# Performance work log

Measured on AMD Instinct MI355X. Metric: run time of the kernel, lower is better.

The kernel has to match this reference:

```python
import jax, jax.numpy as jnp
import numpy as np

D = 1024  # input_dim


def setup_inputs() -> dict:
    key = jax.random.key(0)
    ks = jax.random.split(key, 7)
    s = 1.0 / np.sqrt(D)
    x = jax.random.normal(ks[0], (4, 2048, D), dtype=jnp.float32)
    Wq = jax.random.uniform(ks[1], (D, D), jnp.float32, -s, s)
    bq = jax.random.uniform(ks[2], (D,), jnp.float32, -s, s)
    Wk = jax.random.uniform(ks[3], (D, D), jnp.float32, -s, s)
    bk = jax.random.uniform(ks[4], (D,), jnp.float32, -s, s)
    Wv = jax.random.uniform(ks[5], (D, D), jnp.float32, -s, s)
    bv = jax.random.uniform(ks[6], (D,), jnp.float32, -s, s)
    return {"x": x, "Wq": Wq, "bq": bq, "Wk": Wk, "bk": bk, "Wv": Wv, "bv": bv}


def reference(x, Wq, bq, Wk, bk, Wv, bv):
    # nn.Linear: x @ W.T + b
    q = jnp.einsum('bsd,ed->bse', x, Wq) + bq
    k = jnp.einsum('bsd,ed->bse', x, Wk) + bk
    v = jnp.einsum('bsd,ed->bse', x, Wv) + bv
    scale = 1.0 / jnp.sqrt(jnp.asarray(x.shape[-1], x.dtype))
    scores = jnp.einsum('bqe,bke->bqk', q, k) * scale  # [B,S,S]
    weights = jax.nn.softmax(scores, axis=-1)
    return jnp.einsum('bqk,bke->bqe', weights, v)
```

## Files before the change

kernel.cpp:

```cpp
#include <hip/hip_runtime.h>
#include <hip/hip_bf16.h>
#include <stdint.h>


typedef float f32x4 __attribute__((ext_vector_type(4)));
typedef short s16x8 __attribute__((ext_vector_type(8)));

__device__ __forceinline__ uint16_t f2bf(float f) {
    uint32_t u = __float_as_uint(f);
    u += 0x7fffu + ((u >> 16) & 1u);
    return (uint16_t)(u >> 16);
}

#define GLOAD16(gp, lp)                                                  \
    __builtin_amdgcn_global_load_lds(                                    \
        (const __attribute__((address_space(1))) uint32_t*)(gp),         \
        (__attribute__((address_space(3))) uint32_t*)(lp), 16, 0, 0)


__global__ __launch_bounds__(256, 2) void proj_qkv(
    const uint16_t* __restrict__ xb, const uint16_t* __restrict__ wqb,
    const uint16_t* __restrict__ wkb, const uint16_t* __restrict__ wvb,
    const float* __restrict__ bq, const float* __restrict__ bk,
    const float* __restrict__ bv,
    uint16_t* __restrict__ qb, uint16_t* __restrict__ kb,
    uint16_t* __restrict__ vtb)
{
    __shared__ __attribute__((aligned(16))) uint16_t As[128 * 64];
    __shared__ __attribute__((aligned(16))) uint16_t Bs1[128 * 64];
    __shared__ __attribute__((aligned(16))) uint16_t Bs2[128 * 64];

    const int id = blockIdx.x;
    const bool qk = id < 512;

    const int t = threadIdx.x;
    const int wave = t >> 6, lane = t & 63;
    const int wm = (wave >> 1) * 64, wn = (wave & 1) * 64;
    const int lr = lane & 15;
    const int lr7 = lr & 7;

    long long row0, col0;
    const uint16_t *A, *B1, *B2;
    if (qk) {
        row0 = (long long)(id >> 3) * 128;
        col0 = (long long)(id & 7) * 128;
        A = xb; B1 = wqb; B2 = wkb;
    } else {
        const int vid = id - 512;
        row0 = (long long)(vid & 7) * 128;
        col0 = (long long)(vid >> 3) * 128;
        A = wvb; B1 = xb; B2 = nullptr;
    }

    const uint16_t* gA[4]; const uint16_t* gB1[4]; const uint16_t* gB2[4];
    uint16_t* lA[4]; uint16_t* lB1[4]; uint16_t* lB2[4];
#pragma unroll
    for (int p = 0; p < 4; ++p) {
        const int cs = p * 256 + wave * 64 + lane;
        const int rr = cs >> 3;
        const int kc = ((cs & 7) ^ (rr & 7)) * 8;
        gA[p]  = A  + (row0 + rr) * 1024 + kc;
        gB1[p] = B1 + (col0 + rr) * 1024 + kc;
        if (qk) gB2[p] = B2 + (col0 + rr) * 1024 + kc;
        lA[p]  = As  + (p * 256 + wave * 64) * 8;
        lB1[p] = Bs1 + (p * 256 + wave * 64) * 8;
        lB2[p] = Bs2 + (p * 256 + wave * 64) * 8;
    }

    f32x4 acc1[4][4] = {};
    f32x4 acc2[4][4] = {};

    for (int k0 = 0; k0 < 1024; k0 += 64) {
#pragma unroll
        for (int p = 0; p < 4; ++p) GLOAD16(gA[p] + k0, lA[p]);
#pragma unroll
        for (int p = 0; p < 4; ++p) GLOAD16(gB1[p] + k0, lB1[p]);
        if (qk) {
#pragma unroll
            for (int p = 0; p < 4; ++p) GLOAD16(gB2[p] + k0, lB2[p]);
        }
        __syncthreads();

#pragma unroll
        for (int kk = 0; kk < 2; ++kk) {
            const int lka = ((kk * 4 + (lane >> 4)) ^ lr7) * 8;
            s16x8 a[4], b[4];
#pragma unroll
            for (int i = 0; i < 4; ++i)
                a[i] = *(const s16x8*)(As + (wm + i * 16 + lr) * 64 + lka);
#pragma unroll
            for (int j = 0; j < 4; ++j)
                b[j] = *(const s16x8*)(Bs1 + (wn + j * 16 + lr) * 64 + lka);
#pragma unroll
            for (int i = 0; i < 4; ++i)
#pragma unroll
                for (int j = 0; j < 4; ++j)
                    acc1[i][j] = __builtin_amdgcn_mfma_f32_16x16x32_bf16(
                        a[i], b[j], acc1[i][j], 0, 0, 0);
            if (qk) {
#pragma unroll
                for (int j = 0; j < 4; ++j)
                    b[j] = *(const s16x8*)(Bs2 + (wn + j * 16 + lr) * 64 + lka);
#pragma unroll
                for (int i = 0; i < 4; ++i)
#pragma unroll
                    for (int j = 0; j < 4; ++j)
                        acc2[i][j] = __builtin_amdgcn_mfma_f32_16x16x32_bf16(
                            a[i], b[j], acc2[i][j], 0, 0, 0);
            }
        }
        __syncthreads();
    }

    const int rbase = wm + (lane >> 4) * 4;
    const int cbase = wn + lr;
    if (qk) {
#pragma unroll
        for (int i = 0; i < 4; ++i)
#pragma unroll
            for (int rr = 0; rr < 4; ++rr) {
                const long long row = row0 + rbase + i * 16 + rr;
#pragma unroll
                for (int j = 0; j < 4; ++j) {
                    const long long col = col0 + cbase + j * 16;
                    qb[row * 1024 + col] = f2bf((acc1[i][j][rr] + bq[col]) * 0.03125f);
                    kb[row * 1024 + col] = f2bf(acc2[i][j][rr] + bk[col]);
                }
            }
    } else {
#pragma unroll
        for (int i = 0; i < 4; ++i)
#pragma unroll
            for (int rr = 0; rr < 4; ++rr) {
                const long long row = row0 + rbase + i * 16 + rr;
                const float bb = bv[row];
#pragma unroll
                for (int j = 0; j < 4; ++j) {
                    const long long col = col0 + cbase + j * 16;
                    vtb[row * 8192 + col] = f2bf(acc1[i][j][rr] + bb);
                }
            }
    }
}

__global__ __launch_bounds__(256, 2) void gemm_exp(
    const uint16_t* __restrict__ Q, const uint16_t* __restrict__ Km,
    uint16_t* __restrict__ P, float* __restrict__ sums)
{
    __shared__ __attribute__((aligned(16))) uint16_t As[128 * 64];
    __shared__ __attribute__((aligned(16))) uint16_t Bs1[128 * 64];
    __shared__ __attribute__((aligned(16))) uint16_t Bs2[128 * 64];

    const int z = blockIdx.z;
    const uint16_t* Ab = Q  + (long long)z * 2048 * 1024;
    const uint16_t* Bb = Km + (long long)z * 2048 * 1024;
    uint16_t* Cb = P + (long long)z * 2048 * 2048;
    float* ax = sums + (long long)z * 2048;

    const int t = threadIdx.x;
    const int wave = t >> 6, lane = t & 63;
    const int wm = (wave >> 1) * 64, wn = (wave & 1) * 64;
    const int lr = lane & 15;
    const int lr7 = lr & 7;
    const long long row0  = (long long)blockIdx.x * 128;
    const long long col0a = (long long)blockIdx.y * 256;
    const long long col0b = col0a + 128;

    const uint16_t* gA[4]; const uint16_t* gB1[4]; const uint16_t* gB2[4];
    uint16_t* lA[4]; uint16_t* lB1[4]; uint16_t* lB2[4];
#pragma unroll
    for (int p = 0; p < 4; ++p) {
        const int cs = p * 256 + wave * 64 + lane;
        const int rr = cs >> 3;
        const int kc = ((cs & 7) ^ (rr & 7)) * 8;
        gA[p]  = Ab + (row0  + rr) * 1024 + kc;
        gB1[p] = Bb + (col0a + rr) * 1024 + kc;
        gB2[p] = Bb + (col0b + rr) * 1024 + kc;
        lA[p]  = As  + (p * 256 + wave * 64) * 8;
        lB1[p] = Bs1 + (p * 256 + wave * 64) * 8;
        lB2[p] = Bs2 + (p * 256 + wave * 64) * 8;
    }

    f32x4 acc1[4][4] = {};
    f32x4 acc2[4][4] = {};

    for (int k0 = 0; k0 < 1024; k0 += 64) {
#pragma unroll
        for (int p = 0; p < 4; ++p) GLOAD16(gA[p] + k0, lA[p]);
#pragma unroll
        for (int p = 0; p < 4; ++p) GLOAD16(gB1[p] + k0, lB1[p]);
#pragma unroll
        for (int p = 0; p < 4; ++p) GLOAD16(gB2[p] + k0, lB2[p]);
        __syncthreads();

#pragma unroll
        for (int kk = 0; kk < 2; ++kk) {
            const int lka = ((kk * 4 + (lane >> 4)) ^ lr7) * 8;
            s16x8 a[4], b[4];
#pragma unroll
            for (int i = 0; i < 4; ++i)
                a[i] = *(const s16x8*)(As + (wm + i * 16 + lr) * 64 + lka);
#pragma unroll
            for (int j = 0; j < 4; ++j)
                b[j] = *(const s16x8*)(Bs1 + (wn + j * 16 + lr) * 64 + lka);
#pragma unroll
            for (int i = 0; i < 4; ++i)
#pragma unroll
                for (int j = 0; j < 4; ++j)
                    acc1[i][j] = __builtin_amdgcn_mfma_f32_16x16x32_bf16(
                        a[i], b[j], acc1[i][j], 0, 0, 0);
#pragma unroll
            for (int j = 0; j < 4; ++j)
                b[j] = *(const s16x8*)(Bs2 + (wn + j * 16 + lr) * 64 + lka);
#pragma unroll
            for (int i = 0; i < 4; ++i)
#pragma unroll
                for (int j = 0; j < 4; ++j)
                    acc2[i][j] = __builtin_amdgcn_mfma_f32_16x16x32_bf16(
                        a[i], b[j], acc2[i][j], 0, 0, 0);
        }
        __syncthreads();
    }

    const int rbase = wm + (lane >> 4) * 4;
    const int cbase = wn + lr;
#pragma unroll
    for (int i = 0; i < 4; ++i)
#pragma unroll
        for (int rr = 0; rr < 4; ++rr) {
            const long long row = row0 + rbase + i * 16 + rr;
            float s = 0.f;
#pragma unroll
            for (int j = 0; j < 4; ++j) {
                const long long ca = col0a + cbase + j * 16;
                const long long cb2 = col0b + cbase + j * 16;
                const float va = __expf(acc1[i][j][rr]);
                const float vb = __expf(acc2[i][j][rr]);
                Cb[row * 2048 + ca]  = f2bf(va);
                Cb[row * 2048 + cb2] = f2bf(vb);
                s += va + vb;
            }
            s += __shfl_xor(s, 1);
            s += __shfl_xor(s, 2);
            s += __shfl_xor(s, 4);
            s += __shfl_xor(s, 8);
            if (lr == 0) atomicAdd(&ax[row], s);
        }
}

__global__ __launch_bounds__(256, 2) void gemm_pv(
    const uint16_t* __restrict__ P, const uint16_t* __restrict__ Vt,
    float* __restrict__ Out, const float* __restrict__ sums)
{
    __shared__ __attribute__((aligned(16))) uint16_t As[128 * 64];
    __shared__ __attribute__((aligned(16))) uint16_t Bs[128 * 64];

    const int z = blockIdx.z;
    const uint16_t* Ab = P + (long long)z * 2048 * 2048;
    const uint16_t* Bb = Vt + (long long)z * 2048;
    float* Cb = Out + (long long)z * 2048 * 1024;
    const float* ax = sums + (long long)z * 2048;

    const int t = threadIdx.x;
    const int wave = t >> 6, lane = t & 63;
    const int wm = (wave >> 1) * 64, wn = (wave & 1) * 64;
    const int lr = lane & 15;
    const int lr7 = lr & 7;
    const long long row0 = (long long)blockIdx.x * 128;
    const long long col0 = (long long)blockIdx.y * 128;

    const uint16_t* gA[4]; const uint16_t* gB[4];
    uint16_t* lA[4]; uint16_t* lB[4];
#pragma unroll
    for (int p = 0; p < 4; ++p) {
        const int cs = p * 256 + wave * 64 + lane;
        const int rr = cs >> 3;
        const int kc = ((cs & 7) ^ (rr & 7)) * 8;
        gA[p] = Ab + (row0 + rr) * 2048 + kc;
        gB[p] = Bb + (col0 + rr) * 8192 + kc;
        lA[p] = As + (p * 256 + wave * 64) * 8;
        lB[p] = Bs + (p * 256 + wave * 64) * 8;
    }

    f32x4 acc[4][4] = {};

    for (int k0 = 0; k0 < 2048; k0 += 64) {
#pragma unroll
        for (int p = 0; p < 4; ++p) GLOAD16(gA[p] + k0, lA[p]);
#pragma unroll
        for (int p = 0; p < 4; ++p) GLOAD16(gB[p] + k0, lB[p]);
        __syncthreads();

#pragma unroll
        for (int kk = 0; kk < 2; ++kk) {
            const int lka = ((kk * 4 + (lane >> 4)) ^ lr7) * 8;
            s16x8 a[4], b[4];
#pragma unroll
            for (int i = 0; i < 4; ++i)
                a[i] = *(const s16x8*)(As + (wm + i * 16 + lr) * 64 + lka);
#pragma unroll
            for (int j = 0; j < 4; ++j)
                b[j] = *(const s16x8*)(Bs + (wn + j * 16 + lr) * 64 + lka);
#pragma unroll
            for (int i = 0; i < 4; ++i)
#pragma unroll
                for (int j = 0; j < 4; ++j)
                    acc[i][j] = __builtin_amdgcn_mfma_f32_16x16x32_bf16(
                        a[i], b[j], acc[i][j], 0, 0, 0);
        }
        __syncthreads();
    }

    const int rbase = wm + (lane >> 4) * 4;
    const int cbase = wn + lr;
#pragma unroll
    for (int i = 0; i < 4; ++i)
#pragma unroll
        for (int rr = 0; rr < 4; ++rr) {
            const long long row = row0 + rbase + i * 16 + rr;
            const float linv = __builtin_amdgcn_rcpf(ax[row]);
#pragma unroll
            for (int j = 0; j < 4; ++j) {
                const long long col = col0 + cbase + j * 16;
                Cb[row * 1024 + col] = acc[i][j][rr] * linv;
            }
        }
}

__global__ void cast_all(const float* __restrict__ x, const float* __restrict__ Wq,
                         const float* __restrict__ Wk, const float* __restrict__ Wv,
                         uint16_t* __restrict__ xb, uint16_t* __restrict__ wqb,
                         uint16_t* __restrict__ wkb, uint16_t* __restrict__ wvb,
                         float* __restrict__ sums) {
    const int b = blockIdx.x;
    const float* in;
    uint16_t* out;
    int i;
    if (b < 8192)       { in = x;  out = xb;  i = b * 256 + threadIdx.x; }
    else if (b < 9216)  { in = Wq; out = wqb; i = (b - 8192) * 256 + threadIdx.x; }
    else if (b < 10240) { in = Wk; out = wkb; i = (b - 9216) * 256 + threadIdx.x; }
    else if (b < 11264) { in = Wv; out = wvb; i = (b - 10240) * 256 + threadIdx.x; }
    else {
        int j = (b - 11264) * 256 + threadIdx.x;
        ((float4*)sums)[j] = make_float4(0.f, 0.f, 0.f, 0.f);
        return;
    }
    float4 v = ((const float4*)in)[i];
    ushort4 o = make_ushort4(f2bf(v.x), f2bf(v.y), f2bf(v.z), f2bf(v.w));
    ((ushort4*)out)[i] = o;
}

extern "C" void kernel_launch(void* const* d_in, const int* in_sizes, int n_in,
                              void* d_out, int out_size, void* d_ws, size_t ws_size,
                              hipStream_t stream) {
    const float* x  = (const float*)d_in[0];
    const float* Wq = (const float*)d_in[1];
    const float* bq = (const float*)d_in[2];
    const float* Wk = (const float*)d_in[3];
    const float* bk = (const float*)d_in[4];
    const float* Wv = (const float*)d_in[5];
    const float* bv = (const float*)d_in[6];

    uint8_t* w = (uint8_t*)d_ws;
    uint16_t* xb  = (uint16_t*)w; w += (size_t)8192 * 1024 * 2;
    uint16_t* wqb = (uint16_t*)w; w += (size_t)1024 * 1024 * 2;
    uint16_t* wkb = (uint16_t*)w; w += (size_t)1024 * 1024 * 2;
    uint16_t* wvb = (uint16_t*)w; w += (size_t)1024 * 1024 * 2;
    uint16_t* qb  = (uint16_t*)w; w += (size_t)8192 * 1024 * 2;
    uint16_t* kb  = (uint16_t*)w; w += (size_t)8192 * 1024 * 2;
    uint16_t* vtb = (uint16_t*)w; w += (size_t)8192 * 1024 * 2;
    uint16_t* pb  = (uint16_t*)w; w += (size_t)4 * 2048 * 2048 * 2;
    float*    sums = (float*)w;  w += (size_t)8192 * 4;

    cast_all<<<dim3(11272), dim3(256), 0, stream>>>(x, Wq, Wk, Wv,
                                                    xb, wqb, wkb, wvb, sums);
    proj_qkv<<<dim3(1024), 256, 0, stream>>>(xb, wqb, wkb, wvb, bq, bk, bv,
                                             qb, kb, vtb);
    gemm_exp<<<dim3(16, 8, 4), 256, 0, stream>>>(qb, kb, pb, sums);
    gemm_pv<<<dim3(16, 8, 4), 256, 0, stream>>>(pb, vtb, (float*)d_out, sums);
}
```

Before: 229.7 us.

## Replace GEMM kernels with shared 8-wave double-buffered pipelined GEMM core

Introduces a templated gemm8 core using 512-thread blocks (8 waves), double-buffered LDS with global_load_lds prefetch two tiles ahead, explicit vmcnt waits, split barriers and s_setprio around MFMA clusters. All four GEMM stages (Q/K projection, V^T projection, QK^T+exp, PV) are rebuilt on it with larger 256x256 or 128x256 tiles, and the fused QKV projection is split into separate QK and V kernels. The aim is to overlap memory loads with MFMA work and raise data reuse per block. In exchange it uses more LDS and registers, adds many barriers per k-step, and adds one kernel launch.

```diff
diff --git a/kernel.cpp b/kernel.cpp
--- a/kernel.cpp
+++ b/kernel.cpp
@@ -1,5 +1,4 @@
 #include <hip/hip_runtime.h>
-#include <hip/hip_bf16.h>
 #include <stdint.h>
 
 
@@ -17,228 +16,256 @@
         (const __attribute__((address_space(1))) uint32_t*)(gp),         \
         (__attribute__((address_space(3))) uint32_t*)(lp), 16, 0, 0)
 
-
-__global__ __launch_bounds__(256, 2) void proj_qkv(
-    const uint16_t* __restrict__ xb, const uint16_t* __restrict__ wqb,
-    const uint16_t* __restrict__ wkb, const uint16_t* __restrict__ wvb,
-    const float* __restrict__ bq, const float* __restrict__ bk,
-    const float* __restrict__ bv,
-    uint16_t* __restrict__ qb, uint16_t* __restrict__ kb,
-    uint16_t* __restrict__ vtb)
-{
-    __shared__ __attribute__((aligned(16))) uint16_t As[128 * 64];
-    __shared__ __attribute__((aligned(16))) uint16_t Bs1[128 * 64];
-    __shared__ __attribute__((aligned(16))) uint16_t Bs2[128 * 64];
-
-    const int id = blockIdx.x;
-    const bool qk = id < 512;
-
-    const int t = threadIdx.x;
-    const int wave = t >> 6, lane = t & 63;
-    const int wm = (wave >> 1) * 64, wn = (wave & 1) * 64;
-    const int lr = lane & 15;
-    const int lr7 = lr & 7;
-
-    long long row0, col0;
-    const uint16_t *A, *B1, *B2;
-    if (qk) {
-        row0 = (long long)(id >> 3) * 128;
-        col0 = (long long)(id & 7) * 128;
-        A = xb; B1 = wqb; B2 = wkb;
-    } else {
-        const int vid = id - 512;
-        row0 = (long long)(vid & 7) * 128;
-        col0 = (long long)(vid >> 3) * 128;
-        A = wvb; B1 = xb; B2 = nullptr;
-    }
-
-    const uint16_t* gA[4]; const uint16_t* gB1[4]; const uint16_t* gB2[4];
-    uint16_t* lA[4]; uint16_t* lB1[4]; uint16_t* lB2[4];
-#pragma unroll
-    for (int p = 0; p < 4; ++p) {
-        const int cs = p * 256 + wave * 64 + lane;
+#define FENCE() asm volatile("" ::: "memory")
+#define BAR() do { FENCE(); __builtin_amdgcn_s_barrier(); FENCE(); } while (0)
+
+template <int N> __device__ __forceinline__ void waitv() {
+    if constexpr (N == 8)      asm volatile("s_waitcnt vmcnt(8)" ::: "memory");
+    else if constexpr (N == 6) asm volatile("s_waitcnt vmcnt(6)" ::: "memory");
+    else                       asm volatile("s_waitcnt vmcnt(0)" ::: "memory");
+}
+
+template <int MFRAG>
+__device__ __forceinline__ void gemm8(
+    uint16_t* lds,
+    const uint16_t* __restrict__ Ag, const long long lda,
+    const uint16_t* __restrict__ Bg, const long long ldb,
+    const int NT, f32x4 (&acc)[MFRAG][4])
+{
+    constexpr int BM   = MFRAG * 32;
+    constexpr int AGL  = BM / 64;
+    constexpr int MH   = MFRAG / 2;
+    constexpr int SLOT = (BM + 256) * 64;
+    constexpr int VMN  = AGL + 4;
+
+    const int tid  = threadIdx.x;
+    const int wave = tid >> 6, lane = tid & 63;
+    const int lr   = lane & 15, hi = lane >> 4, lr7 = lane & 7;
+
+    const uint16_t* gA[AGL]; int lA[AGL];
+    const uint16_t* gB[4];   int lB[4];
+#pragma unroll
+    for (int p = 0; p < AGL; ++p) {
+        const int cs = p * 512 + tid;
         const int rr = cs >> 3;
         const int kc = ((cs & 7) ^ (rr & 7)) * 8;
-        gA[p]  = A  + (row0 + rr) * 1024 + kc;
-        gB1[p] = B1 + (col0 + rr) * 1024 + kc;
-        if (qk) gB2[p] = B2 + (col0 + rr) * 1024 + kc;
-        lA[p]  = As  + (p * 256 + wave * 64) * 8;
-        lB1[p] = Bs1 + (p * 256 + wave * 64) * 8;
-        lB2[p] = Bs2 + (p * 256 + wave * 64) * 8;
+        gA[p] = Ag + (long long)rr * lda + kc;
+        lA[p] = (p * 512 + wave * 64) * 8;
     }
-
-    f32x4 acc1[4][4] = {};
-    f32x4 acc2[4][4] = {};
-
-    for (int k0 = 0; k0 < 1024; k0 += 64) {
-#pragma unroll
-        for (int p = 0; p < 4; ++p) GLOAD16(gA[p] + k0, lA[p]);
-#pragma unroll
-        for (int p = 0; p < 4; ++p) GLOAD16(gB1[p] + k0, lB1[p]);
-        if (qk) {
-#pragma unroll
-            for (int p = 0; p < 4; ++p) GLOAD16(gB2[p] + k0, lB2[p]);
-        }
-        __syncthreads();
-
-#pragma unroll
-        for (int kk = 0; kk < 2; ++kk) {
-            const int lka = ((kk * 4 + (lane >> 4)) ^ lr7) * 8;
-            s16x8 a[4], b[4];
-#pragma unroll
-            for (int i = 0; i < 4; ++i)
-                a[i] = *(const s16x8*)(As + (wm + i * 16 + lr) * 64 + lka);
-#pragma unroll
-            for (int j = 0; j < 4; ++j)
-                b[j] = *(const s16x8*)(Bs1 + (wn + j * 16 + lr) * 64 + lka);
-#pragma unroll
-            for (int i = 0; i < 4; ++i)
-#pragma unroll
-                for (int j = 0; j < 4; ++j)
-                    acc1[i][j] = __builtin_amdgcn_mfma_f32_16x16x32_bf16(
-                        a[i], b[j], acc1[i][j], 0, 0, 0);
-            if (qk) {
-#pragma unroll
-                for (int j = 0; j < 4; ++j)
-                    b[j] = *(const s16x8*)(Bs2 + (wn + j * 16 + lr) * 64 + lka);
-#pragma unroll
-                for (int i = 0; i < 4; ++i)
-#pragma unroll
-                    for (int j = 0; j < 4; ++j)
-                        acc2[i][j] = __builtin_amdgcn_mfma_f32_16x16x32_bf16(
-                            a[i], b[j], acc2[i][j], 0, 0, 0);
+#pragma unroll
+    for (int p = 0; p < 4; ++p) {
+        const int cs = p * 512 + tid;
+        const int rr = cs >> 3;
+        const int kc = ((cs & 7) ^ (rr & 7)) * 8;
+        gB[p] = Bg + (long long)rr * ldb + kc;
+        lB[p] = BM * 64 + (p * 512 + wave * 64) * 8;
+    }
+
+    const int wrow = (wave >> 2) * (MFRAG * 16);
+    const int wcol = (wave & 3) * 64;
+    const int arow = (wrow + lr) * 64;
+    const int brow = BM * 64 + (wcol + lr) * 64;
+    const int koff0 = (hi ^ lr7) * 8;
+    const int koff1 = ((4 + hi) ^ lr7) * 8;
+
+#pragma unroll
+    for (int p = 0; p < AGL; ++p) GLOAD16(gA[p], lds + lA[p]);
+#pragma unroll
+    for (int p = 0; p < 4;  ++p) GLOAD16(gB[p], lds + lB[p]);
+#pragma unroll
+    for (int p = 0; p < AGL; ++p) GLOAD16(gA[p] + 64, lds + SLOT + lA[p]);
+#pragma unroll
+    for (int p = 0; p < 4;  ++p) GLOAD16(gB[p] + 64, lds + SLOT + lB[p]);
+    waitv<VMN>();
+    BAR();
+
+    s16x8 a[MH][2], b0[2][2], b1[2][2];
+
+    for (int t = 0; t < NT; ++t) {
+        uint16_t* L = lds + (t & 1) * SLOT;
+        const int k0 = (t + 2) * 64;
+        const bool pf = (t + 2) < NT;
+
+#pragma unroll
+        for (int i = 0; i < MH; ++i) {
+            a[i][0] = *(const s16x8*)(L + arow + i * 1024 + koff0);
+            a[i][1] = *(const s16x8*)(L + arow + i * 1024 + koff1);
+        }
+#pragma unroll
+        for (int j = 0; j < 2; ++j) {
+            b0[j][0] = *(const s16x8*)(L + brow + j * 1024 + koff0);
+            b0[j][1] = *(const s16x8*)(L + brow + j * 1024 + koff1);
+        }
+        BAR();
+        __builtin_amdgcn_s_setprio(1);
+#pragma unroll
+        for (int kk = 0; kk < 2; ++kk)
+#pragma unroll
+            for (int i = 0; i < MH; ++i)
+#pragma unroll
+                for (int j = 0; j < 2; ++j)
+                    acc[i][j] = __builtin_amdgcn_mfma_f32_16x16x32_bf16(
+                        a[i][kk], b0[j][kk], acc[i][j], 0, 0, 0);
+        __builtin_amdgcn_s_setprio(0);
+        BAR();
+
+#pragma unroll
+        for (int j = 0; j < 2; ++j) {
+            b1[j][0] = *(const s16x8*)(L + brow + (2 + j) * 1024 + koff0);
+            b1[j][1] = *(const s16x8*)(L + brow + (2 + j) * 1024 + koff1);
+        }
+        BAR();
+        __builtin_amdgcn_s_setprio(1);
+#pragma unroll
+        for (int kk = 0; kk < 2; ++kk)
+#pragma unroll
+            for (int i = 0; i < MH; ++i)
+#pragma unroll
+                for (int j = 0; j < 2; ++j)
+                    acc[i][2 + j] = __builtin_amdgcn_mfma_f32_16x16x32_bf16(
+                        a[i][kk], b1[j][kk], acc[i][2 + j], 0, 0, 0);
+        __builtin_amdgcn_s_setprio(0);
+        BAR();
+
+#pragma unroll
+        for (int i = 0; i < MH; ++i) {
+            a[i][0] = *(const s16x8*)(L + arow + (MH + i) * 1024 + koff0);
+            a[i][1] = *(const s16x8*)(L + arow + (MH + i) * 1024 + koff1);
+        }
+        if (pf) {
+#pragma unroll
+            for (int p = 0; p < 4; ++p) GLOAD16(gB[p] + k0, L + lB[p]);
+        }
+        BAR();
+        __builtin_amdgcn_s_setprio(1);
+#pragma unroll
+        for (int kk = 0; kk < 2; ++kk)
+#pragma unroll
+            for (int i = 0; i < MH; ++i)
+#pragma unroll
+                for (int j = 0; j < 2; ++j)
+                    acc[MH + i][2 + j] = __builtin_amdgcn_mfma_f32_16x16x32_bf16(
+                        a[i][kk], b1[j][kk], acc[MH + i][2 + j], 0, 0, 0);
+        __builtin_amdgcn_s_setprio(0);
+        BAR();
+
+        if (pf) {
+#pragma unroll
+            for (int p = 0; p < AGL; ++p) GLOAD16(gA[p] + k0, L + lA[p]);
+        }
+        BAR();
+        __builtin_amdgcn_s_setprio(1);
+#pragma unroll
+        for (int kk = 0; kk < 2; ++kk)
+#pragma unroll
+            for (int i = 0; i < MH; ++i)
+#pragma unroll
+                for (int j = 0; j < 2; ++j)
+                    acc[MH + i][j] = __builtin_amdgcn_mfma_f32_16x16x32_bf16(
+                        a[i][kk], b0[j][kk], acc[MH + i][j], 0, 0, 0);
+        __builtin_amdgcn_s_setprio(0);
+        if (pf) waitv<VMN>(); else waitv<0>();
+        BAR();
+    }
+}
+
+__global__ __launch_bounds__(512, 2) void qk_proj8(
+    const uint16_t* __restrict__ xb, const uint16_t* __restrict__ wqb,
+    const uint16_t* __restrict__ wkb, const float* __restrict__ bq,
+    const float* __restrict__ bk, uint16_t* __restrict__ qb,
+    uint16_t* __restrict__ kb)
+{
+    __shared__ __attribute__((aligned(16))) uint16_t lds[2 * 512 * 64];
+    const long long row0 = (long long)blockIdx.x * 256;
+    const bool isQ = blockIdx.y < 4;
+    const long long col0 = (long long)(blockIdx.y & 3) * 256;
+    const uint16_t* W = isQ ? wqb : wkb;
+
+    f32x4 acc[8][4] = {};
+    gemm8<8>(lds, xb + row0 * 1024, 1024, W + col0 * 1024, 1024, 16, acc);
+
+    const float* bias = isQ ? bq : bk;
+    uint16_t* out = isQ ? qb : kb;
+    const float scale = isQ ? 0.03125f : 1.0f;
+
+    const int tid = threadIdx.x;
+    const int wave = tid >> 6, lane = tid & 63;
+    const int lr = lane & 15, hi = lane >> 4;
+    const int wrow = (wave >> 2) * 128, wcol = (wave & 3) * 64;
+#pragma unroll
+    for (int i = 0; i < 8; ++i)
+#pragma unroll
+        for (int rr = 0; rr < 4; ++rr) {
+            const long long row = row0 + wrow + i * 16 + hi * 4 + rr;
+#pragma unroll
+            for (int j = 0; j < 4; ++j) {
+                const long long col = col0 + wcol + j * 16 + lr;
+                out[row * 1024 + col] = f2bf((acc[i][j][rr] + bias[col]) * scale);
             }
         }
-        __syncthreads();
-    }
-
-    const int rbase = wm + (lane >> 4) * 4;
-    const int cbase = wn + lr;
-    if (qk) {
-#pragma unroll
-        for (int i = 0; i < 4; ++i)
-#pragma unroll
-            for (int rr = 0; rr < 4; ++rr) {
-                const long long row = row0 + rbase + i * 16 + rr;
-#pragma unroll
-                for (int j = 0; j < 4; ++j) {
-                    const long long col = col0 + cbase + j * 16;
-                    qb[row * 1024 + col] = f2bf((acc1[i][j][rr] + bq[col]) * 0.03125f);
-                    kb[row * 1024 + col] = f2bf(acc2[i][j][rr] + bk[col]);
-                }
+}
+
+__global__ __launch_bounds__(512, 2) void vt_proj8(
+    const uint16_t* __restrict__ xb, const uint16_t* __restrict__ wvb,
+    const float* __restrict__ bv, uint16_t* __restrict__ vtb)
+{
+    __shared__ __attribute__((aligned(16))) uint16_t lds[2 * 384 * 64];
+    const long long row0 = (long long)blockIdx.x * 128;
+    const long long col0 = (long long)blockIdx.y * 256;
+
+    f32x4 acc[4][4] = {};
+    gemm8<4>(lds, wvb + row0 * 1024, 1024, xb + col0 * 1024, 1024, 16, acc);
+
+    const int tid = threadIdx.x;
+    const int wave = tid >> 6, lane = tid & 63;
+    const int lr = lane & 15, hi = lane >> 4;
+    const int wrow = (wave >> 2) * 64, wcol = (wave & 3) * 64;
+#pragma unroll
+    for (int i = 0; i < 4; ++i)
+#pragma unroll
+        for (int rr = 0; rr < 4; ++rr) {
+            const long long row = row0 + wrow + i * 16 + hi * 4 + rr;
+            const float bb = bv[row];
+#pragma unroll
+            for (int j = 0; j < 4; ++j) {
+                const long long col = col0 + wcol + j * 16 + lr;
+                vtb[row * 8192 + col] = f2bf(acc[i][j][rr] + bb);
             }
-    } else {
-#pragma unroll
-        for (int i = 0; i < 4; ++i)
-#pragma unroll
-            for (int rr = 0; rr < 4; ++rr) {
-                const long long row = row0 + rbase + i * 16 + rr;
-                const float bb = bv[row];
-#pragma unroll
-                for (int j = 0; j < 4; ++j) {
-                    const long long col = col0 + cbase + j * 16;
-                    vtb[row * 8192 + col] = f2bf(acc1[i][j][rr] + bb);
-                }
-            }
-    }
-}
-
-__global__ __launch_bounds__(256, 2) void gemm_exp(
+        }
+}
+
+__global__ __launch_bounds__(512, 2) void gemm_exp8(
     const uint16_t* __restrict__ Q, const uint16_t* __restrict__ Km,
     uint16_t* __restrict__ P, float* __restrict__ sums)
 {
-    __shared__ __attribute__((aligned(16))) uint16_t As[128 * 64];
-    __shared__ __attribute__((aligned(16))) uint16_t Bs1[128 * 64];
-    __shared__ __attribute__((aligned(16))) uint16_t Bs2[128 * 64];
-
+    __shared__ __attribute__((aligned(16))) uint16_t lds[2 * 512 * 64];
     const int z = blockIdx.z;
-    const uint16_t* Ab = Q  + (long long)z * 2048 * 1024;
-    const uint16_t* Bb = Km + (long long)z * 2048 * 1024;
+    const long long row0 = (long long)blockIdx.x * 256;
+    const long long col0 = (long long)blockIdx.y * 256;
+    const uint16_t* Ab = Q  + (long long)z * 2048 * 1024 + row0 * 1024;
+    const uint16_t* Bb = Km + (long long)z * 2048 * 1024 + col0 * 1024;
     uint16_t* Cb = P + (long long)z * 2048 * 2048;
     float* ax = sums + (long long)z * 2048;
 
-    const int t = threadIdx.x;
-    const int wave = t >> 6, lane = t & 63;
-    const int wm = (wave >> 1) * 64, wn = (wave & 1) * 64;
-    const int lr = lane & 15;
-    const int lr7 = lr & 7;
-    const long long row0  = (long long)blockIdx.x * 128;
-    const long long col0a = (long long)blockIdx.y * 256;
-    const long long col0b = col0a + 128;
-
-    const uint16_t* gA[4]; const uint16_t* gB1[4]; const uint16_t* gB2[4];
-    uint16_t* lA[4]; uint16_t* lB1[4]; uint16_t* lB2[4];
-#pragma unroll
-    for (int p = 0; p < 4; ++p) {
-        const int cs = p * 256 + wave * 64 + lane;
-        const int rr = cs >> 3;
-        const int kc = ((cs & 7) ^ (rr & 7)) * 8;
-        gA[p]  = Ab + (row0  + rr) * 1024 + kc;
-        gB1[p] = Bb + (col0a + rr) * 1024 + kc;
-        gB2[p] = Bb + (col0b + rr) * 1024 + kc;
-        lA[p]  = As  + (p * 256 + wave * 64) * 8;
-        lB1[p] = Bs1 + (p * 256 + wave * 64) * 8;
-        lB2[p] = Bs2 + (p * 256 + wave * 64) * 8;
-    }
-
-    f32x4 acc1[4][4] = {};
-    f32x4 acc2[4][4] = {};
-
-    for (int k0 = 0; k0 < 1024; k0 += 64) {
-#pragma unroll
-        for (int p = 0; p < 4; ++p) GLOAD16(gA[p] + k0, lA[p]);
-#pragma unroll
-        for (int p = 0; p < 4; ++p) GLOAD16(gB1[p] + k0, lB1[p]);
-#pragma unroll
-        for (int p = 0; p < 4; ++p) GLOAD16(gB2[p] + k0, lB2[p]);
-        __syncthreads();
-
-#pragma unroll
-        for (int kk = 0; kk < 2; ++kk) {
-            const int lka = ((kk * 4 + (lane >> 4)) ^ lr7) * 8;
-            s16x8 a[4], b[4];
-#pragma unroll
-            for (int i = 0; i < 4; ++i)
-                a[i] = *(const s16x8*)(As + (wm + i * 16 + lr) * 64 + lka);
-#pragma unroll
-            for (int j = 0; j < 4; ++j)
-                b[j] = *(const s16x8*)(Bs1 + (wn + j * 16 + lr) * 64 + lka);
-#pragma unroll
-            for (int i = 0; i < 4; ++i)
-#pragma unroll
-                for (int j = 0; j < 4; ++j)
-                    acc1[i][j] = __builtin_amdgcn_mfma_f32_16x16x32_bf16(
-                        a[i], b[j], acc1[i][j], 0, 0, 0);
-#pragma unroll
-            for (int j = 0; j < 4; ++j)
-                b[j] = *(const s16x8*)(Bs2 + (wn + j * 16 + lr) * 64 + lka);
-#pragma unroll
-            for (int i = 0; i < 4; ++i)
-#pragma unroll
-                for (int j = 0; j < 4; ++j)
-                    acc2[i][j] = __builtin_amdgcn_mfma_f32_16x16x32_bf16(
-                        a[i], b[j], acc2[i][j], 0, 0, 0);
-        }
-        __syncthreads();
-    }
-
-    const int rbase = wm + (lane >> 4) * 4;
-    const int cbase = wn + lr;
-#pragma unroll
-    for (int i = 0; i < 4; ++i)
+    f32x4 acc[8][4] = {};
+    gemm8<8>(lds, Ab, 1024, Bb, 1024, 16, acc);
+
+    const int tid = threadIdx.x;
+    const int wave = tid >> 6, lane = tid & 63;
+    const int lr = lane & 15, hi = lane >> 4;
+    const int wrow = (wave >> 2) * 128, wcol = (wave & 3) * 64;
+#pragma unroll
+    for (int i = 0; i < 8; ++i)
 #pragma unroll
         for (int rr = 0; rr < 4; ++rr) {
-            const long long row = row0 + rbase + i * 16 + rr;
+            const long long row = row0 + wrow + i * 16 + hi * 4 + rr;
             float s = 0.f;
 #pragma unroll
             for (int j = 0; j < 4; ++j) {
-                const long long ca = col0a + cbase + j * 16;
-                const long long cb2 = col0b + cbase + j * 16;
-                const float va = __expf(acc1[i][j][rr]);
-                const float vb = __expf(acc2[i][j][rr]);
-                Cb[row * 2048 + ca]  = f2bf(va);
-                Cb[row * 2048 + cb2] = f2bf(vb);
-                s += va + vb;
+                const long long col = col0 + wcol + j * 16 + lr;
+                const float v = __expf(acc[i][j][rr]);
+                Cb[row * 2048 + col] = f2bf(v);
+                s += v;
             }
             s += __shfl_xor(s, 1);
             s += __shfl_xor(s, 2);
@@ -248,80 +275,35 @@
         }
 }
 
-__global__ __launch_bounds__(256, 2) void gemm_pv(
+__global__ __launch_bounds__(512, 2) void gemm_pv8(
     const uint16_t* __restrict__ P, const uint16_t* __restrict__ Vt,
     float* __restrict__ Out, const float* __restrict__ sums)
 {
-    __shared__ __attribute__((aligned(16))) uint16_t As[128 * 64];
-    __shared__ __attribute__((aligned(16))) uint16_t Bs[128 * 64];
-
+    __shared__ __attribute__((aligned(16))) uint16_t lds[2 * 384 * 64];
     const int z = blockIdx.z;
-    const uint16_t* Ab = P + (long long)z * 2048 * 2048;
-    const uint16_t* Bb = Vt + (long long)z * 2048;
+    const long long row0 = (long long)blockIdx.x * 128;
+    const long long col0 = (long long)blockIdx.y * 256;
+    const uint16_t* Ab = P + (long long)z * 2048 * 2048 + row0 * 2048;
+    const uint16_t* Bb = Vt + col0 * 8192 + (long long)z * 2048;
     float* Cb = Out + (long long)z * 2048 * 1024;
     const float* ax = sums + (long long)z * 2048;
 
-    const int t = threadIdx.x;
-    const int wave = t >> 6, lane = t & 63;
-    const int wm = (wave >> 1) * 64, wn = (wave & 1) * 64;
-    const int lr = lane & 15;
-    const int lr7 = lr & 7;
-    const long long row0 = (long long)blockIdx.x * 128;
-    const long long col0 = (long long)blockIdx.y * 128;
-
-    const uint16_t* gA[4]; const uint16_t* gB[4];
-    uint16_t* lA[4]; uint16_t* lB[4];
-#pragma unroll
-    for (int p = 0; p < 4; ++p) {
-        const int cs = p * 256 + wave * 64 + lane;
-        const int rr = cs >> 3;
-        const int kc = ((cs & 7) ^ (rr & 7)) * 8;
-        gA[p] = Ab + (row0 + rr) * 2048 + kc;
-        gB[p] = Bb + (col0 + rr) * 8192 + kc;
-        lA[p] = As + (p * 256 + wave * 64) * 8;
-        lB[p] = Bs + (p * 256 + wave * 64) * 8;
-    }
-
     f32x4 acc[4][4] = {};
-
-    for (int k0 = 0; k0 < 2048; k0 += 64) {
-#pragma unroll
-        for (int p = 0; p < 4; ++p) GLOAD16(gA[p] + k0, lA[p]);
-#pragma unroll
-        for (int p = 0; p < 4; ++p) GLOAD16(gB[p] + k0, lB[p]);
-        __syncthreads();
-
-#pragma unroll
-        for (int kk = 0; kk < 2; ++kk) {
-            const int lka = ((kk * 4 + (lane >> 4)) ^ lr7) * 8;
-            s16x8 a[4], b[4];
-#pragma unroll
-            for (int i = 0; i < 4; ++i)
-                a[i] = *(const s16x8*)(As + (wm + i * 16 + lr) * 64 + lka);
-#pragma unroll
-            for (int j = 0; j < 4; ++j)
-                b[j] = *(const s16x8*)(Bs + (wn + j * 16 + lr) * 64 + lka);
-#pragma unroll
-            for (int i = 0; i < 4; ++i)
-#pragma unroll
-                for (int j = 0; j < 4; ++j)
-                    acc[i][j] = __builtin_amdgcn_mfma_f32_16x16x32_bf16(
-                        a[i], b[j], acc[i][j], 0, 0, 0);
-        }
-        __syncthreads();
-    }
-
-    const int rbase = wm + (lane >> 4) * 4;
-    const int cbase = wn + lr;
+    gemm8<4>(lds, Ab, 2048, Bb, 8192, 32, acc);
+
+    const int tid = threadIdx.x;
+    const int wave = tid >> 6, lane = tid & 63;
+    const int lr = lane & 15, hi = lane >> 4;
+    const int wrow = (wave >> 2) * 64, wcol = (wave & 3) * 64;
 #pragma unroll
     for (int i = 0; i < 4; ++i)
 #pragma unroll
         for (int rr = 0; rr < 4; ++rr) {
-            const long long row = row0 + rbase + i * 16 + rr;
+            const long long row = row0 + wrow + i * 16 + hi * 4 + rr;
             const float linv = __builtin_amdgcn_rcpf(ax[row]);
 #pragma unroll
             for (int j = 0; j < 4; ++j) {
-                const long long col = col0 + cbase + j * 16;
+                const long long col = col0 + wcol + j * 16 + lr;
                 Cb[row * 1024 + col] = acc[i][j][rr] * linv;
             }
         }
@@ -374,8 +356,8 @@
 
     cast_all<<<dim3(11272), dim3(256), 0, stream>>>(x, Wq, Wk, Wv,
                                                     xb, wqb, wkb, wvb, sums);
-    proj_qkv<<<dim3(1024), 256, 0, stream>>>(xb, wqb, wkb, wvb, bq, bk, bv,
-                                             qb, kb, vtb);
-    gemm_exp<<<dim3(16, 8, 4), 256, 0, stream>>>(qb, kb, pb, sums);
-    gemm_pv<<<dim3(16, 8, 4), 256, 0, stream>>>(pb, vtb, (float*)d_out, sums);
-}
+    qk_proj8<<<dim3(32, 8), dim3(512), 0, stream>>>(xb, wqb, wkb, bq, bk, qb, kb);
+    vt_proj8<<<dim3(8, 32), dim3(512), 0, stream>>>(xb, wvb, bv, vtb);
+    gemm_exp8<<<dim3(8, 8, 4), dim3(512), 0, stream>>>(qb, kb, pb, sums);
+    gemm_pv8<<<dim3(16, 4, 4), dim3(512), 0, stream>>>(pb, vtb, (float*)d_out, sums);
+}
```

New measurement: 240.1 us. 1.05x slower.

## Unify GEMMs into a shared 128x128 core with XCD-aware block swizzle

Applied to the files above, without the earlier changes.

Factors the three GEMM kernels into one shared 128x128 tile routine and splits the dual-B tiles (Q+K together, two K column blocks together) into separate single-B blocks. This cuts LDS per block from 48KB to 32KB and accumulator registers by half, so launch bounds rise to 3 blocks per CU. Grids are flattened and remapped with an XCD swizzle so neighbouring tiles share each chiplet's L2. In exchange, the A tile is loaded from global memory twice as often, because it is no longer shared across two B tiles.

```diff
diff --git a/kernel.cpp b/kernel.cpp
--- a/kernel.cpp
+++ b/kernel.cpp
@@ -1,5 +1,4 @@
 #include <hip/hip_runtime.h>
-#include <hip/hip_bf16.h>
 #include <stdint.h>
 
 
@@ -17,8 +16,62 @@
         (const __attribute__((address_space(1))) uint32_t*)(gp),         \
         (__attribute__((address_space(3))) uint32_t*)(lp), 16, 0, 0)
 
-
-__global__ __launch_bounds__(256, 2) void proj_qkv(
+__device__ __forceinline__ int xcd_swz(int b, int nwg) {
+    return (b & 7) * (nwg >> 3) + (b >> 3);
+}
+
+__device__ __forceinline__ void gemm_core(
+    uint16_t* __restrict__ As, uint16_t* __restrict__ Bs,
+    const uint16_t* __restrict__ Ag, const long long lda,
+    const uint16_t* __restrict__ Bg, const long long ldb,
+    const int NT, f32x4 (&acc)[4][4])
+{
+    const int t = threadIdx.x;
+    const int wave = t >> 6, lane = t & 63;
+    const int wm = (wave >> 1) * 64, wn = (wave & 1) * 64;
+    const int lr = lane & 15, hi = lane >> 4, lr7 = lane & 7;
+
+    const uint16_t* gA[4]; const uint16_t* gB[4];
+    uint16_t* lA[4]; uint16_t* lB[4];
+#pragma unroll
+    for (int p = 0; p < 4; ++p) {
+        const int cs = p * 256 + t;
+        const int rr = cs >> 3;
+        const int kc = ((cs & 7) ^ (rr & 7)) * 8;
+        gA[p] = Ag + (long long)rr * lda + kc;
+        gB[p] = Bg + (long long)rr * ldb + kc;
+        lA[p] = As + (p * 256 + wave * 64) * 8;
+        lB[p] = Bs + (p * 256 + wave * 64) * 8;
+    }
+
+    for (int k0 = 0; k0 < NT * 64; k0 += 64) {
+#pragma unroll
+        for (int p = 0; p < 4; ++p) GLOAD16(gA[p] + k0, lA[p]);
+#pragma unroll
+        for (int p = 0; p < 4; ++p) GLOAD16(gB[p] + k0, lB[p]);
+        __syncthreads();
+#pragma unroll
+        for (int kk = 0; kk < 2; ++kk) {
+            const int lka = ((kk * 4 + hi) ^ lr7) * 8;
+            s16x8 a[4], b[4];
+#pragma unroll
+            for (int i = 0; i < 4; ++i)
+                a[i] = *(const s16x8*)(As + (wm + i * 16 + lr) * 64 + lka);
+#pragma unroll
+            for (int j = 0; j < 4; ++j)
+                b[j] = *(const s16x8*)(Bs + (wn + j * 16 + lr) * 64 + lka);
+#pragma unroll
+            for (int i = 0; i < 4; ++i)
+#pragma unroll
+                for (int j = 0; j < 4; ++j)
+                    acc[i][j] = __builtin_amdgcn_mfma_f32_16x16x32_bf16(
+                        a[i], b[j], acc[i][j], 0, 0, 0);
+        }
+        __syncthreads();
+    }
+}
+
+__global__ __launch_bounds__(256, 3) void proj_all(
     const uint16_t* __restrict__ xb, const uint16_t* __restrict__ wqb,
     const uint16_t* __restrict__ wkb, const uint16_t* __restrict__ wvb,
     const float* __restrict__ bq, const float* __restrict__ bk,
@@ -27,218 +80,94 @@
     uint16_t* __restrict__ vtb)
 {
     __shared__ __attribute__((aligned(16))) uint16_t As[128 * 64];
-    __shared__ __attribute__((aligned(16))) uint16_t Bs1[128 * 64];
-    __shared__ __attribute__((aligned(16))) uint16_t Bs2[128 * 64];
-
-    const int id = blockIdx.x;
-    const bool qk = id < 512;
-
-    const int t = threadIdx.x;
-    const int wave = t >> 6, lane = t & 63;
-    const int wm = (wave >> 1) * 64, wn = (wave & 1) * 64;
-    const int lr = lane & 15;
-    const int lr7 = lr & 7;
-
-    long long row0, col0;
-    const uint16_t *A, *B1, *B2;
-    if (qk) {
-        row0 = (long long)(id >> 3) * 128;
-        col0 = (long long)(id & 7) * 128;
-        A = xb; B1 = wqb; B2 = wkb;
+    __shared__ __attribute__((aligned(16))) uint16_t Bs[128 * 64];
+
+    const int id = xcd_swz(blockIdx.x, 1536);
+    const int t = threadIdx.x;
+    const int wave = t >> 6, lane = t & 63;
+    const int wm = (wave >> 1) * 64, wn = (wave & 1) * 64;
+    const int lr = lane & 15, hi = lane >> 4;
+
+    f32x4 acc[4][4] = {};
+
+    if (id < 1024) {
+        const int mat = id >> 9;
+        const long long row0 = (long long)((id >> 3) & 63) * 128;
+        const long long col0 = (long long)(id & 7) * 128;
+        const uint16_t* W = mat ? wkb : wqb;
+        gemm_core(As, Bs, xb + row0 * 1024, 1024, W + col0 * 1024, 1024, 16, acc);
+
+        const float* bias = mat ? bk : bq;
+        uint16_t* out = mat ? kb : qb;
+        const float scale = mat ? 1.0f : 0.03125f;
+#pragma unroll
+        for (int i = 0; i < 4; ++i)
+#pragma unroll
+            for (int rr = 0; rr < 4; ++rr) {
+                const long long row = row0 + wm + i * 16 + hi * 4 + rr;
+#pragma unroll
+                for (int j = 0; j < 4; ++j) {
+                    const long long col = col0 + wn + j * 16 + lr;
+                    out[row * 1024 + col] = f2bf((acc[i][j][rr] + bias[col]) * scale);
+                }
+            }
     } else {
-        const int vid = id - 512;
-        row0 = (long long)(vid & 7) * 128;
-        col0 = (long long)(vid >> 3) * 128;
-        A = wvb; B1 = xb; B2 = nullptr;
-    }
-
-    const uint16_t* gA[4]; const uint16_t* gB1[4]; const uint16_t* gB2[4];
-    uint16_t* lA[4]; uint16_t* lB1[4]; uint16_t* lB2[4];
-#pragma unroll
-    for (int p = 0; p < 4; ++p) {
-        const int cs = p * 256 + wave * 64 + lane;
-        const int rr = cs >> 3;
-        const int kc = ((cs & 7) ^ (rr & 7)) * 8;
-        gA[p]  = A  + (row0 + rr) * 1024 + kc;
-        gB1[p] = B1 + (col0 + rr) * 1024 + kc;
-        if (qk) gB2[p] = B2 + (col0 + rr) * 1024 + kc;
-        lA[p]  = As  + (p * 256 + wave * 64) * 8;
-        lB1[p] = Bs1 + (p * 256 + wave * 64) * 8;
-        lB2[p] = Bs2 + (p * 256 + wave * 64) * 8;
-    }
-
-    f32x4 acc1[4][4] = {};
-    f32x4 acc2[4][4] = {};
-
-    for (int k0 = 0; k0 < 1024; k0 += 64) {
-#pragma unroll
-        for (int p = 0; p < 4; ++p) GLOAD16(gA[p] + k0, lA[p]);
-#pragma unroll
-        for (int p = 0; p < 4; ++p) GLOAD16(gB1[p] + k0, lB1[p]);
-        if (qk) {
-#pragma unroll
-            for (int p = 0; p < 4; ++p) GLOAD16(gB2[p] + k0, lB2[p]);
-        }
-        __syncthreads();
-
-#pragma unroll
-        for (int kk = 0; kk < 2; ++kk) {
-            const int lka = ((kk * 4 + (lane >> 4)) ^ lr7) * 8;
-            s16x8 a[4], b[4];
-#pragma unroll
-            for (int i = 0; i < 4; ++i)
-                a[i] = *(const s16x8*)(As + (wm + i * 16 + lr) * 64 + lka);
-#pragma unroll
-            for (int j = 0; j < 4; ++j)
-                b[j] = *(const s16x8*)(Bs1 + (wn + j * 16 + lr) * 64 + lka);
-#pragma unroll
-            for (int i = 0; i < 4; ++i)
-#pragma unroll
-                for (int j = 0; j < 4; ++j)
-                    acc1[i][j] = __builtin_amdgcn_mfma_f32_16x16x32_bf16(
-                        a[i], b[j], acc1[i][j], 0, 0, 0);
-            if (qk) {
-#pragma unroll
-                for (int j = 0; j < 4; ++j)
-                    b[j] = *(const s16x8*)(Bs2 + (wn + j * 16 + lr) * 64 + lka);
-#pragma unroll
-                for (int i = 0; i < 4; ++i)
-#pragma unroll
-                    for (int j = 0; j < 4; ++j)
-                        acc2[i][j] = __builtin_amdgcn_mfma_f32_16x16x32_bf16(
-                            a[i], b[j], acc2[i][j], 0, 0, 0);
-            }
-        }
-        __syncthreads();
-    }
-
-    const int rbase = wm + (lane >> 4) * 4;
-    const int cbase = wn + lr;
-    if (qk) {
+        const int vid = id - 1024;
+        const long long row0 = (long long)(vid & 7) * 128;
+        const long long col0 = (long long)(vid >> 3) * 128;
+        gemm_core(As, Bs, wvb + row0 * 1024, 1024, xb + col0 * 1024, 1024, 16, acc);
 #pragma unroll
         for (int i = 0; i < 4; ++i)
 #pragma unroll
             for (int rr = 0; rr < 4; ++rr) {
-                const long long row = row0 + rbase + i * 16 + rr;
+                const long long row = row0 + wm + i * 16 + hi * 4 + rr;
+                const float bb = bv[row];
 #pragma unroll
                 for (int j = 0; j < 4; ++j) {
-                    const long long col = col0 + cbase + j * 16;
-                    qb[row * 1024 + col] = f2bf((acc1[i][j][rr] + bq[col]) * 0.03125f);
-                    kb[row * 1024 + col] = f2bf(acc2[i][j][rr] + bk[col]);
+                    const long long col = col0 + wn + j * 16 + lr;
+                    vtb[row * 8192 + col] = f2bf(acc[i][j][rr] + bb);
                 }
             }
-    } else {
-#pragma unroll
-        for (int i = 0; i < 4; ++i)
-#pragma unroll
-            for (int rr = 0; rr < 4; ++rr) {
-                const long long row = row0 + rbase + i * 16 + rr;
-                const float bb = bv[row];
-#pragma unroll
-                for (int j = 0; j < 4; ++j) {
-                    const long long col = col0 + cbase + j * 16;
-                    vtb[row * 8192 + col] = f2bf(acc1[i][j][rr] + bb);
-                }
-            }
-    }
-}
-
-__global__ __launch_bounds__(256, 2) void gemm_exp(
+    }
+}
+
+__global__ __launch_bounds__(256, 3) void gemm_exp(
     const uint16_t* __restrict__ Q, const uint16_t* __restrict__ Km,
     uint16_t* __restrict__ P, float* __restrict__ sums)
 {
     __shared__ __attribute__((aligned(16))) uint16_t As[128 * 64];
-    __shared__ __attribute__((aligned(16))) uint16_t Bs1[128 * 64];
-    __shared__ __attribute__((aligned(16))) uint16_t Bs2[128 * 64];
-
-    const int z = blockIdx.z;
-    const uint16_t* Ab = Q  + (long long)z * 2048 * 1024;
-    const uint16_t* Bb = Km + (long long)z * 2048 * 1024;
+    __shared__ __attribute__((aligned(16))) uint16_t Bs[128 * 64];
+
+    const int id = xcd_swz(blockIdx.x, 1024);
+    const int z = id >> 8;
+    const int rem = id & 255;
+    const long long row0 = (long long)(rem & 15) * 128;
+    const long long col0 = (long long)(rem >> 4) * 128;
+
+    const uint16_t* Ab = Q  + (long long)z * 2048 * 1024 + row0 * 1024;
+    const uint16_t* Bb = Km + (long long)z * 2048 * 1024 + col0 * 1024;
     uint16_t* Cb = P + (long long)z * 2048 * 2048;
     float* ax = sums + (long long)z * 2048;
 
-    const int t = threadIdx.x;
-    const int wave = t >> 6, lane = t & 63;
-    const int wm = (wave >> 1) * 64, wn = (wave & 1) * 64;
-    const int lr = lane & 15;
-    const int lr7 = lr & 7;
-    const long long row0  = (long long)blockIdx.x * 128;
-    const long long col0a = (long long)blockIdx.y * 256;
-    const long long col0b = col0a + 128;
-
-    const uint16_t* gA[4]; const uint16_t* gB1[4]; const uint16_t* gB2[4];
-    uint16_t* lA[4]; uint16_t* lB1[4]; uint16_t* lB2[4];
-#pragma unroll
-    for (int p = 0; p < 4; ++p) {
-        const int cs = p * 256 + wave * 64 + lane;
-        const int rr = cs >> 3;
-        const int kc = ((cs & 7) ^ (rr & 7)) * 8;
-        gA[p]  = Ab + (row0  + rr) * 1024 + kc;
-        gB1[p] = Bb + (col0a + rr) * 1024 + kc;
-        gB2[p] = Bb + (col0b + rr) * 1024 + kc;
-        lA[p]  = As  + (p * 256 + wave * 64) * 8;
-        lB1[p] = Bs1 + (p * 256 + wave * 64) * 8;
-        lB2[p] = Bs2 + (p * 256 + wave * 64) * 8;
-    }
-
-    f32x4 acc1[4][4] = {};
-    f32x4 acc2[4][4] = {};
-
-    for (int k0 = 0; k0 < 1024; k0 += 64) {
-#pragma unroll
-        for (int p = 0; p < 4; ++p) GLOAD16(gA[p] + k0, lA[p]);
-#pragma unroll
-        for (int p = 0; p < 4; ++p) GLOAD16(gB1[p] + k0, lB1[p]);
-#pragma unroll
-        for (int p = 0; p < 4; ++p) GLOAD16(gB2[p] + k0, lB2[p]);
-        __syncthreads();
-
-#pragma unroll
-        for (int kk = 0; kk < 2; ++kk) {
-            const int lka = ((kk * 4 + (lane >> 4)) ^ lr7) * 8;
-            s16x8 a[4], b[4];
-#pragma unroll
-            for (int i = 0; i < 4; ++i)
-                a[i] = *(const s16x8*)(As + (wm + i * 16 + lr) * 64 + lka);
-#pragma unroll
-            for (int j = 0; j < 4; ++j)
-                b[j] = *(const s16x8*)(Bs1 + (wn + j * 16 + lr) * 64 + lka);
-#pragma unroll
-            for (int i = 0; i < 4; ++i)
-#pragma unroll
-                for (int j = 0; j < 4; ++j)
-                    acc1[i][j] = __builtin_amdgcn_mfma_f32_16x16x32_bf16(
-                        a[i], b[j], acc1[i][j], 0, 0, 0);
-#pragma unroll
-            for (int j = 0; j < 4; ++j)
-                b[j] = *(const s16x8*)(Bs2 + (wn + j * 16 + lr) * 64 + lka);
-#pragma unroll
-            for (int i = 0; i < 4; ++i)
-#pragma unroll
-                for (int j = 0; j < 4; ++j)
-                    acc2[i][j] = __builtin_amdgcn_mfma_f32_16x16x32_bf16(
-                        a[i], b[j], acc2[i][j], 0, 0, 0);
-        }
-        __syncthreads();
-    }
-
-    const int rbase = wm + (lane >> 4) * 4;
-    const int cbase = wn + lr;
+    f32x4 acc[4][4] = {};
+    gemm_core(As, Bs, Ab, 1024, Bb, 1024, 16, acc);
+
+    const int t = threadIdx.x;
+    const int wave = t >> 6, lane = t & 63;
+    const int wm = (wave >> 1) * 64, wn = (wave & 1) * 64;
+    const int lr = lane & 15, hi = lane >> 4;
 #pragma unroll
     for (int i = 0; i < 4; ++i)
 #pragma unroll
         for (int rr = 0; rr < 4; ++rr) {
-            const long long row = row0 + rbase + i * 16 + rr;
+            const long long row = row0 + wm + i * 16 + hi * 4 + rr;
             float s = 0.f;
 #pragma unroll
             for (int j = 0; j < 4; ++j) {
-                const long long ca = col0a + cbase + j * 16;
-                const long long cb2 = col0b + cbase + j * 16;
-                const float va = __expf(acc1[i][j][rr]);
-                const float vb = __expf(acc2[i][j][rr]);
-                Cb[row * 2048 + ca]  = f2bf(va);
-                Cb[row * 2048 + cb2] = f2bf(vb);
-                s += va + vb;
+                const long long col = col0 + wn + j * 16 + lr;
+                const float v = __expf(acc[i][j][rr]);
+                Cb[row * 2048 + col] = f2bf(v);
+                s += v;
             }
             s += __shfl_xor(s, 1);
             s += __shfl_xor(s, 2);
@@ -248,80 +177,40 @@
         }
 }
 
-__global__ __launch_bounds__(256, 2) void gemm_pv(
+__global__ __launch_bounds__(256, 3) void gemm_pv(
     const uint16_t* __restrict__ P, const uint16_t* __restrict__ Vt,
     float* __restrict__ Out, const float* __restrict__ sums)
 {
     __shared__ __attribute__((aligned(16))) uint16_t As[128 * 64];
     __shared__ __attribute__((aligned(16))) uint16_t Bs[128 * 64];
 
-    const int z = blockIdx.z;
-    const uint16_t* Ab = P + (long long)z * 2048 * 2048;
-    const uint16_t* Bb = Vt + (long long)z * 2048;
+    const int id = xcd_swz(blockIdx.x, 512);
+    const int z = id >> 7;
+    const int rem = id & 127;
+    const long long row0 = (long long)(rem & 15) * 128;
+    const long long col0 = (long long)(rem >> 4) * 128;
+
+    const uint16_t* Ab = P + (long long)z * 2048 * 2048 + row0 * 2048;
+    const uint16_t* Bb = Vt + col0 * 8192 + (long long)z * 2048;
     float* Cb = Out + (long long)z * 2048 * 1024;
     const float* ax = sums + (long long)z * 2048;
 
-    const int t = threadIdx.x;
-    const int wave = t >> 6, lane = t & 63;
-    const int wm = (wave >> 1) * 64, wn = (wave & 1) * 64;
-    const int lr = lane & 15;
-    const int lr7 = lr & 7;
-    const long long row0 = (long long)blockIdx.x * 128;
-    const long long col0 = (long long)blockIdx.y * 128;
-
-    const uint16_t* gA[4]; const uint16_t* gB[4];
-    uint16_t* lA[4]; uint16_t* lB[4];
-#pragma unroll
-    for (int p = 0; p < 4; ++p) {
-        const int cs = p * 256 + wave * 64 + lane;
-        const int rr = cs >> 3;
-        const int kc = ((cs & 7) ^ (rr & 7)) * 8;
-        gA[p] = Ab + (row0 + rr) * 2048 + kc;
-        gB[p] = Bb + (col0 + rr) * 8192 + kc;
-        lA[p] = As + (p * 256 + wave * 64) * 8;
-        lB[p] = Bs + (p * 256 + wave * 64) * 8;
-    }
-
     f32x4 acc[4][4] = {};
-
-    for (int k0 = 0; k0 < 2048; k0 += 64) {
-#pragma unroll
-        for (int p = 0; p < 4; ++p) GLOAD16(gA[p] + k0, lA[p]);
-#pragma unroll
-        for (int p = 0; p < 4; ++p) GLOAD16(gB[p] + k0, lB[p]);
-        __syncthreads();
-
-#pragma unroll
-        for (int kk = 0; kk < 2; ++kk) {
-            const int lka = ((kk * 4 + (lane >> 4)) ^ lr7) * 8;
-            s16x8 a[4], b[4];
-#pragma unroll
-            for (int i = 0; i < 4; ++i)
-                a[i] = *(const s16x8*)(As + (wm + i * 16 + lr) * 64 + lka);
-#pragma unroll
-            for (int j = 0; j < 4; ++j)
-                b[j] = *(const s16x8*)(Bs + (wn + j * 16 + lr) * 64 + lka);
-#pragma unroll
-            for (int i = 0; i < 4; ++i)
-#pragma unroll
-                for (int j = 0; j < 4; ++j)
-                    acc[i][j] = __builtin_amdgcn_mfma_f32_16x16x32_bf16(
-                        a[i], b[j], acc[i][j], 0, 0, 0);
-        }
-        __syncthreads();
-    }
-
-    const int rbase = wm + (lane >> 4) * 4;
-    const int cbase = wn + lr;
+    gemm_core(As, Bs, Ab, 2048, Bb, 8192, 32, acc);
+
+    const int t = threadIdx.x;
+    const int wave = t >> 6, lane = t & 63;
+    const int wm = (wave >> 1) * 64, wn = (wave & 1) * 64;
+    const int lr = lane & 15, hi = lane >> 4;
 #pragma unroll
     for (int i = 0; i < 4; ++i)
 #pragma unroll
         for (int rr = 0; rr < 4; ++rr) {
-            const long long row = row0 + rbase + i * 16 + rr;
+            const long long row = row0 + wm + i * 16 + hi * 4 + rr;
             const float linv = __builtin_amdgcn_rcpf(ax[row]);
 #pragma unroll
             for (int j = 0; j < 4; ++j) {
-                const long long col = col0 + cbase + j * 16;
+                const long long col = col0 + wn + j * 16 + lr;
                 Cb[row * 1024 + col] = acc[i][j][rr] * linv;
             }
         }
@@ -374,8 +263,8 @@
 
     cast_all<<<dim3(11272), dim3(256), 0, stream>>>(x, Wq, Wk, Wv,
                                                     xb, wqb, wkb, wvb, sums);
-    proj_qkv<<<dim3(1024), 256, 0, stream>>>(xb, wqb, wkb, wvb, bq, bk, bv,
-                                             qb, kb, vtb);
-    gemm_exp<<<dim3(16, 8, 4), 256, 0, stream>>>(qb, kb, pb, sums);
-    gemm_pv<<<dim3(16, 8, 4), 256, 0, stream>>>(pb, vtb, (float*)d_out, sums);
-}
+    proj_all<<<dim3(1536), dim3(256), 0, stream>>>(xb, wqb, wkb, wvb,
+                                                   bq, bk, bv, qb, kb, vtb);
+    gemm_exp<<<dim3(1024), dim3(256), 0, stream>>>(qb, kb, pb, sums);
+    gemm_pv<<<dim3(512), dim3(256), 0, stream>>>(pb, vtb, (float*)d_out, sums);
+}
```

Result: faster. 224.9 us (-2.1%).
